# Optimization experiments

Hardware: AMD Instinct MI355X
Metric: run time of the kernel (lower is better)

Reference implementation:

```python
import jax, jax.numpy as jnp
import numpy as np

HI, WI = 56, 56
HO, WO = HI // 2, WI // 2
N_IN, N_OUT = HI * WI, HO * WO
DIM_IN, DIM_OUT = 96, 192
HIDDEN = DIM_OUT * 2
NUM_ITERS = 3
LN_EPS = 1e-5


def _build_mask_and_qidx():
    # M_loc: 0 inside 3x3 window around each input token's parent slot, -1e4 outside.
    # qidx: relative-position index in {0..8}, -1 outside window (torch rpb[-1] == rpb[8]).
    mask = np.full((N_IN, N_OUT), -10000.0, dtype=np.float32)
    qidx = np.full((N_IN, N_OUT), -1, dtype=np.int32)
    in_r, in_c = np.meshgrid(np.arange(HI), np.arange(WI), indexing='ij')
    in_r, in_c = in_r.ravel(), in_c.ravel()
    out_r0 = np.clip(in_r // 2, 0, HO - 1)
    out_c0 = np.clip(in_c // 2, 0, WO - 1)
    in_idx = np.arange(N_IN)
    k = 0
    for dr in (-1, 0, 1):
        for dc in (-1, 0, 1):
            out_r = np.clip(out_r0 + dr, 0, HO - 1)
            out_c = np.clip(out_c0 + dc, 0, WO - 1)
            out_idx = out_r * WO + out_c
            mask[in_idx, out_idx] = 0.0
            qidx[in_idx, out_idx] = k
            k += 1
    return jnp.asarray(mask), jnp.asarray(qidx)


def layer_norm(x, g, b):
    mu = jnp.mean(x, axis=-1, keepdims=True)
    var = jnp.var(x, axis=-1, keepdims=True)
    return (x - mu) * jax.lax.rsqrt(var + LN_EPS) * g + b


def setup_inputs() -> dict:
    key = jax.random.key(0)
    ks = jax.random.split(key, 10)
    B = 8
    x = jax.random.normal(ks[0], (B, N_IN, DIM_IN), dtype=jnp.float32)
    # Parameters (torch Linear weight layout [out, in])
    conv_w = jax.random.normal(ks[1], (DIM_OUT, DIM_IN, 3, 3), dtype=jnp.float32) * np.sqrt(2.0 / (DIM_IN * 9))
    q_w = jax.random.normal(ks[2], (DIM_IN, DIM_OUT), dtype=jnp.float32) * (DIM_OUT ** -0.5)
    k_w = jax.random.normal(ks[3], (DIM_IN, DIM_IN), dtype=jnp.float32) * (DIM_IN ** -0.5)
    v_w = jax.random.normal(ks[4], (DIM_OUT, DIM_IN), dtype=jnp.float32) * (DIM_IN ** -0.5)
    mlp_w1 = jax.random.normal(ks[5], (HIDDEN, DIM_OUT), dtype=jnp.float32) * (DIM_OUT ** -0.5)
    mlp_b1 = jnp.zeros((HIDDEN,), dtype=jnp.float32)
    mlp_w2 = jax.random.normal(ks[6], (DIM_OUT, HIDDEN), dtype=jnp.float32) * (HIDDEN ** -0.5)
    mlp_b2 = jnp.zeros((DIM_OUT,), dtype=jnp.float32)
    ln_in_g = jnp.ones((DIM_IN,), jnp.float32); ln_in_b = jnp.zeros((DIM_IN,), jnp.float32)
    ln_out_g = jnp.ones((DIM_OUT,), jnp.float32); ln_out_b = jnp.zeros((DIM_OUT,), jnp.float32)
    ln_attn_g = jnp.ones((DIM_OUT,), jnp.float32); ln_attn_b = jnp.zeros((DIM_OUT,), jnp.float32)
    ln_mlp_g = jnp.ones((DIM_OUT,), jnp.float32); ln_mlp_b = jnp.zeros((DIM_OUT,), jnp.float32)
    tau = jnp.asarray(np.log(DIM_IN ** -0.5), dtype=jnp.float32)
    rpb = jax.random.truncated_normal(ks[7], -2.0, 2.0, (9,), dtype=jnp.float32) * 0.02
    M_loc, qidx = _build_mask_and_qidx()
    return dict(x=x, conv_w=conv_w, q_w=q_w, k_w=k_w, v_w=v_w,
                mlp_w1=mlp_w1, mlp_b1=mlp_b1, mlp_w2=mlp_w2, mlp_b2=mlp_b2,
                ln_in_g=ln_in_g, ln_in_b=ln_in_b, ln_out_g=ln_out_g, ln_out_b=ln_out_b,
                ln_attn_g=ln_attn_g, ln_attn_b=ln_attn_b, ln_mlp_g=ln_mlp_g, ln_mlp_b=ln_mlp_b,
                tau=tau, rpb=rpb, M_loc=M_loc, qidx=qidx)


def reference(x, conv_w, q_w, k_w, v_w, mlp_w1, mlp_b1, mlp_w2, mlp_b2,
              ln_in_g, ln_in_b, ln_out_g, ln_out_b, ln_attn_g, ln_attn_b,
              ln_mlp_g, ln_mlp_b, tau, rpb, M_loc, qidx):
    B = x.shape[0]
    # seed: strided 3x3 conv (stride 2, pad 1), NCHW
    x_img = jnp.transpose(x, (0, 2, 1)).reshape(B, DIM_IN, HI, WI)
    seed = jax.lax.conv_general_dilated(
        x_img, conv_w, window_strides=(2, 2), padding=((1, 1), (1, 1)),
        dimension_numbers=('NCHW', 'OIHW', 'NCHW'))  # [B, dim_out, Ho, Wo]
    x_out = layer_norm(jnp.transpose(seed.reshape(B, DIM_OUT, N_OUT), (0, 2, 1)), ln_out_g, ln_out_b)
    xn = layer_norm(x, ln_in_g, ln_in_b)
    k = xn @ k_w.T  # [B, N_in, dim_in]
    v = xn @ v_w.T  # [B, N_in, dim_out]
    # relative-position bias gather; torch index -1 wraps to 8
    bias = rpb[jnp.where(qidx < 0, qidx + 9, qidx)]  # [N_in, N_out]
    add = bias + M_loc  # fused constant-per-batch additive term
    a_ups = a_down = None
    for _ in range(NUM_ITERS):
        q = layer_norm(x_out, ln_out_g, ln_out_b) @ q_w.T  # [B, N_out, dim_in]
        logits = jnp.einsum('bnd,bmd->bnm', k, q) * jnp.exp(tau) + add
        a_ups = jax.nn.softmax(logits, axis=-1)          # row softmax over slots
        col_sums = jnp.sum(a_ups, axis=1, keepdims=True)  # column renorm (Sinkhorn-like)
        a_down = a_ups / (col_sums + 1e-8)
        updates = jnp.einsum('bnm,bnd->bmd', a_down, v)   # [B, N_out, dim_out]
        x_out = x_out + layer_norm(updates, ln_attn_g, ln_attn_b)
        h = jax.nn.gelu(x_out @ mlp_w1.T + mlp_b1, approximate=False) @ mlp_w2.T + mlp_b2
        x_out = x_out + layer_norm(h, ln_mlp_g, ln_mlp_b)
    return x_out, a_ups, a_down
```

## Files before the change

kernel.cpp:

```cpp
#include <hip/hip_runtime.h>
#include <hip/hip_bf16.h>
#include <math.h>

#define NB 8
#define NIN 3136
#define NOUT 784
#define DIN 96
#define DOUT 192
#define HID 384
#define TOK_IN (NB*NIN)
#define TOK_OUT (NB*NOUT)

__device__ __forceinline__ void window9(int n, int* ms, bool* dup) {
  int r = n / 56, c = n % 56;
  int rb = r >> 1, cb = c >> 1;
  #pragma unroll
  for (int j = 0; j < 9; j++) {
    int ro = rb + (j/3) - 1; ro = ro < 0 ? 0 : (ro > 27 ? 27 : ro);
    int co = cb + (j%3) - 1; co = co < 0 ? 0 : (co > 27 ? 27 : co);
    ms[j] = ro*28 + co;
  }
  #pragma unroll
  for (int j = 0; j < 9; j++) {
    bool d = false;
    #pragma unroll
    for (int i = 0; i < j; i++) d = d || (ms[i] == ms[j]);
    dup[j] = d;
  }
}

__global__ void k_tr(const float* __restrict__ cw, const float* __restrict__ kw,
                     const float* __restrict__ vw, const float* __restrict__ qw,
                     const float* __restrict__ w1, const float* __restrict__ w2,
                     const float* __restrict__ rpb, const int* __restrict__ qidx,
                     float* __restrict__ wct, float* __restrict__ wkv4, float* __restrict__ qw4,
                     float* __restrict__ w1_4, float* __restrict__ w2_4,
                     float* __restrict__ bias9) {
  int i = blockIdx.x * 256 + threadIdx.x;
  if (i < 165888) {
    int q = i & 3; int t1 = i >> 2;
    int co = t1 % 192; int t2 = t1 / 192;
    int kwi = t2 % 3; int t3 = t2 / 3;
    int ci4m = t3 % 6; int t4 = t3 / 6;
    int kh = t4 % 3; int ch = t4 / 3;
    wct[i] = cw[((co*96 + ch*24 + ci4m*4 + q)*3 + kh)*3 + kwi];
  } else if (i < 165888 + 27648) {
    int j = i - 165888; int q = j & 3; int rest = j >> 2;
    int o = rest % 288; int e = (rest / 288)*4 + q;
    wkv4[j] = (o < 96) ? kw[o*96 + e] : vw[(o-96)*96 + e];
  } else if (i < 165888 + 27648 + 18432) {
    int j = i - 165888 - 27648; int q = j & 3; int rest = j >> 2;
    int o = rest % 96; int e = (rest / 96)*4 + q;
    qw4[j] = qw[o*192 + e];
  } else if (i < 165888 + 27648 + 18432 + 73728) {
    int j = i - 165888 - 27648 - 18432; int q = j & 3; int rest = j >> 2;
    int hh = rest % 384; int e = (rest / 384)*4 + q;
    w1_4[j] = w1[hh*192 + e];
  } else if (i < 165888 + 27648 + 18432 + 73728 + 73728) {
    int j = i - 165888 - 27648 - 18432 - 73728; int q = j & 3; int rest = j >> 2;
    int o = rest % 192; int h = (rest / 192)*4 + q;
    w2_4[j] = w2[o*384 + h];
  } else if (i < 165888 + 27648 + 18432 + 73728 + 73728 + 28224) {
    int j = i - 165888 - 27648 - 18432 - 73728 - 73728;
    int j9 = j % 9; int n = j / 9;
    int ms[9]; bool dup[9];
    window9(n, ms, dup);
    bias9[j] = rpb[qidx[(size_t)n*NOUT + ms[j9]]];
  }
}

__global__ __launch_bounds__(224, 4) void k_conv(const float* __restrict__ x,
                                                 const float* __restrict__ wct,
                                                 float* __restrict__ s0, float* __restrict__ s1,
                                                 float* __restrict__ s2, float* __restrict__ s3) {
  __shared__ float xs[3][58][24];
  int ho = blockIdx.x;
  int half = blockIdx.y & 1, ch = blockIdx.y >> 1;
  int b = blockIdx.z;
  int t = threadIdx.x;
  const float* xb0 = x + (size_t)b*NIN*DIN + ch*24;
  for (int i = t; i < 3*58*6; i += 224) {
    int q = i % 6; int rest = i / 6;
    int col = rest % 58; int kh = rest / 58;
    int h = 2*ho - 1 + kh, c = col - 1;
    float4 v = make_float4(0.f,0.f,0.f,0.f);
    if (h >= 0 && h < 56 && c >= 0 && c < 56)
      v = *(const float4*)(xb0 + ((size_t)h*56 + c)*DIN + q*4);
    *(float4*)&xs[kh][col][q*4] = v;
  }
  __syncthreads();
  int ol = t & 31, tg = t >> 5;
  int co = half*96 + ol;
  float acc[4][3];
  #pragma unroll
  for (int i = 0; i < 4; i++) { acc[i][0]=0.f; acc[i][1]=0.f; acc[i][2]=0.f; }
  #pragma unroll
  for (int kh = 0; kh < 3; kh++) {
    const float4* wp = (const float4*)wct + (size_t)(ch*3 + kh)*3456 + co;
    const float* xb = &xs[kh][8*tg][0];
    #pragma unroll
    for (int ci4 = 0; ci4 < 6; ci4++) {
      float4 xr[9];
      #pragma unroll
      for (int c = 0; c < 9; c++) xr[c] = *(const float4*)(xb + c*24);
      #pragma unroll
      for (int kwv = 0; kwv < 3; kwv++) {
        float4 w0 = wp[kwv*192], w1 = wp[kwv*192 + 32], w2 = wp[kwv*192 + 64];
        #pragma unroll
        for (int i = 0; i < 4; i++) {
          float4 xv = xr[2*i + kwv];
          acc[i][0] += xv.x*w0.x + xv.y*w0.y + xv.z*w0.z + xv.w*w0.w;
          acc[i][1] += xv.x*w1.x + xv.y*w1.y + xv.z*w1.z + xv.w*w1.w;
          acc[i][2] += xv.x*w2.x + xv.y*w2.y + xv.z*w2.z + xv.w*w2.w;
        }
      }
      wp += 576; xb += 4;
    }
  }
  float* sp = (ch == 0) ? s0 : (ch == 1) ? s1 : (ch == 2) ? s2 : s3;
  #pragma unroll
  for (int i = 0; i < 4; i++)
    #pragma unroll
    for (int j = 0; j < 3; j++)
      sp[((size_t)b*NOUT + ho*28 + 4*tg + i)*DOUT + co + 32*j] = acc[i][j];
}

__global__ __launch_bounds__(256) void k_lnq(const float* __restrict__ s0, const float* __restrict__ s1,
                                             const float* __restrict__ s2, const float* __restrict__ s3,
                                             const float* __restrict__ qw4,
                                             const float* __restrict__ lng, const float* __restrict__ lnb,
                                             float* __restrict__ xo, float* __restrict__ qb) {
  __shared__ float xt[16][196];
  int tok0 = blockIdx.x * 16;
  int t = threadIdx.x;
  int tok16 = t >> 4, l16 = t & 15;
  size_t base = (size_t)(tok0 + tok16)*DOUT;
  float v[12], s = 0.f, sq = 0.f;
  #pragma unroll
  for (int j = 0; j < 12; j++) {
    int e = l16 + 16*j;
    float vv = s0[base + e] + s1[base + e] + s2[base + e] + s3[base + e];
    v[j] = vv; s += vv; sq += vv*vv;
  }
  #pragma unroll
  for (int off = 8; off; off >>= 1) { s += __shfl_xor(s, off, 16); sq += __shfl_xor(sq, off, 16); }
  float mu = s * (1.f/192.f);
  float var = sq * (1.f/192.f) - mu*mu;
  float rs = rsqrtf(var + 1e-5f);
  float s2a = 0.f, sq2 = 0.f;
  #pragma unroll
  for (int j = 0; j < 12; j++) {
    int e = l16 + 16*j;
    float y = (v[j]-mu)*rs*lng[e] + lnb[e];
    xo[base + e] = y;
    v[j] = y; s2a += y; sq2 += y*y;
  }
  #pragma unroll
  for (int off = 8; off; off >>= 1) { s2a += __shfl_xor(s2a, off, 16); sq2 += __shfl_xor(sq2, off, 16); }
  float mu2 = s2a * (1.f/192.f);
  float var2 = sq2 * (1.f/192.f) - mu2*mu2;
  float rs2 = rsqrtf(var2 + 1e-5f);
  #pragma unroll
  for (int j = 0; j < 12; j++) {
    int e = l16 + 16*j;
    xt[tok16][e] = (v[j]-mu2)*rs2*lng[e] + lnb[e];
  }
  __syncthreads();
  int ol = t & 31, tg = t >> 5;
  float acc[2][3];
  #pragma unroll
  for (int i = 0; i < 2; i++) { acc[i][0]=0.f; acc[i][1]=0.f; acc[i][2]=0.f; }
  const float4* wp = (const float4*)qw4 + ol;
  for (int e4 = 0; e4 < 48; e4++) {
    float4 w0 = wp[0], w1 = wp[32], w2 = wp[64];
    #pragma unroll
    for (int i = 0; i < 2; i++) {
      float4 xv = *(const float4*)&xt[tg*2+i][e4*4];
      acc[i][0] += xv.x*w0.x + xv.y*w0.y + xv.z*w0.z + xv.w*w0.w;
      acc[i][1] += xv.x*w1.x + xv.y*w1.y + xv.z*w1.z + xv.w*w1.w;
      acc[i][2] += xv.x*w2.x + xv.y*w2.y + xv.z*w2.z + xv.w*w2.w;
    }
    wp += 96;
  }
  #pragma unroll
  for (int i = 0; i < 2; i++)
    #pragma unroll
    for (int j = 0; j < 3; j++)
      qb[(size_t)(tok0 + tg*2 + i)*DIN + ol + 32*j] = acc[i][j];
}

__global__ __launch_bounds__(256) void k_kv(const float* __restrict__ x,
                                            const float* __restrict__ wkv4,
                                            const float* __restrict__ lng, const float* __restrict__ lnb,
                                            float* __restrict__ kvb) {
  __shared__ float xt[32][100];
  int tok0 = blockIdx.x * 32;
  int t = threadIdx.x;
  const float4* xp = (const float4*)(x + (size_t)tok0*DIN);
  for (int i = t; i < 32*24; i += 256) {
    int tok = i / 24, q = i % 24;
    *(float4*)&xt[tok][q*4] = xp[i];
  }
  __syncthreads();
  int tok8 = t >> 3, l8 = t & 7;
  float vv[12], s = 0.f, sq = 0.f;
  #pragma unroll
  for (int j = 0; j < 12; j++) {
    float v = xt[tok8][l8 + 8*j];
    vv[j] = v; s += v; sq += v*v;
  }
  #pragma unroll
  for (int off = 4; off; off >>= 1) { s += __shfl_xor(s, off, 8); sq += __shfl_xor(sq, off, 8); }
  float mu = s * (1.f/96.f);
  float var = sq * (1.f/96.f) - mu*mu;
  float rs = rsqrtf(var + 1e-5f);
  #pragma unroll
  for (int j = 0; j < 12; j++) {
    int e = l8 + 8*j;
    xt[tok8][e] = (vv[j]-mu)*rs*lng[e] + lnb[e];
  }
  __syncthreads();
  int ol = t & 31, tg = t >> 5;
  float acc[4][9];
  #pragma unroll
  for (int i = 0; i < 4; i++)
    #pragma unroll
    for (int j = 0; j < 9; j++) acc[i][j] = 0.f;
  const float4* wp = (const float4*)wkv4 + ol;
  for (int e4 = 0; e4 < 24; e4++) {
    float4 w[9];
    #pragma unroll
    for (int j = 0; j < 9; j++) w[j] = wp[32*j];
    #pragma unroll
    for (int i = 0; i < 4; i++) {
      float4 xv = *(const float4*)&xt[tg*4+i][e4*4];
      #pragma unroll
      for (int j = 0; j < 9; j++)
        acc[i][j] += xv.x*w[j].x + xv.y*w[j].y + xv.z*w[j].z + xv.w*w[j].w;
    }
    wp += 288;
  }
  #pragma unroll
  for (int i = 0; i < 4; i++)
    #pragma unroll
    for (int j = 0; j < 9; j++)
      kvb[(size_t)(tok0 + tg*4 + i)*288 + ol + 32*j] = acc[i][j];
}

__global__ __launch_bounds__(256) void k_attn1(const float* __restrict__ kvb,
                                               const float* __restrict__ qb,
                                               const float* __restrict__ tau,
                                               const float* __restrict__ bias9,
                                               float* __restrict__ aups,
                                               float* __restrict__ adown, int zmode) {
  int t = threadIdx.x;
  int half = (t >> 5) & 1, ll = t & 31;
  int tid = blockIdx.x * 8 + (t >> 6) * 2 + half;
  int b = tid / NIN, n = tid % NIN;
  int ms[9]; bool dup[9];
  window9(n, ms, dup);
  const float* kp = kvb + (size_t)tid * 288;
  float k0 = kp[ll], k1 = kp[32 + ll], k2 = kp[64 + ll];
  float et = expf(tau[0]);
  float p[9];
  #pragma unroll
  for (int j = 0; j < 9; j++) {
    const float* qp = qb + (size_t)(b*NOUT + ms[j]) * DIN;
    p[j] = k0 * qp[ll] + k1 * qp[32 + ll] + k2 * qp[64 + ll];
  }
  #pragma unroll
  for (int off = 16; off; off >>= 1)
    #pragma unroll
    for (int j = 0; j < 9; j++) p[j] += __shfl_xor(p[j], off, 32);
  const float* bp = bias9 + (size_t)n*9;
  float lg[9];
  #pragma unroll
  for (int j = 0; j < 9; j++)
    lg[j] = dup[j] ? -1e30f : p[j] * et + bp[j];
  float mx = lg[0];
  #pragma unroll
  for (int j = 1; j < 9; j++) mx = fmaxf(mx, lg[j]);
  float s = 0.f, ex[9];
  #pragma unroll
  for (int j = 0; j < 9; j++) { ex[j] = dup[j] ? 0.f : expf(lg[j] - mx); s += ex[j]; }
  float inv = 1.0f / s;
  if (zmode) {
    float* ap = aups + (size_t)tid*NOUT;
    float* dp = adown + (size_t)tid*NOUT;
    #pragma unroll
    for (int k = 0; k < 25; k++) {
      int e = ll + 32*k;
      if (e < NOUT) {
        float v = 0.f;
        #pragma unroll
        for (int j = 0; j < 9; j++)
          if (!dup[j] && e == ms[j]) v = ex[j] * inv;
        ap[e] = v;
        dp[e] = 0.f;
      }
    }
  } else {
    #pragma unroll
    for (int j = 0; j < 9; j++) {
      if (ll == j && !dup[j])
        aups[(size_t)tid*NOUT + ms[j]] = ex[j] * inv;
    }
  }
}

__global__ __launch_bounds__(192) void k_upd(const float* __restrict__ aups,
                                             const float* __restrict__ kvb,
                                             float* __restrict__ xout,
                                             const float* __restrict__ g,
                                             const float* __restrict__ bb,
                                             float* __restrict__ adown, int wadown) {
  __shared__ float avals[4][64];
  __shared__ float red[4][3][2];
  __shared__ float bc[4][2];
  __shared__ float csv[4];
  int b = blockIdx.z;
  int ro0 = blockIdx.y*2, co0 = blockIdx.x*2;
  int r0 = 2*ro0 - 2; if (r0 < 0) r0 = 0;
  int r1 = 2*ro0 + 5; if (r1 > 55) r1 = 55;
  int c0 = 2*co0 - 2; if (c0 < 0) c0 = 0;
  int c1 = 2*co0 + 5; if (c1 > 55) c1 = 55;
  int nr = r1 - r0 + 1, nc = c1 - c0 + 1, cnt = nr*nc;
  int t = threadIdx.x;
  int m0 = ro0*28 + co0, m1 = m0+1, m2 = m0+28, m3 = m0+29;
  if (t < cnt) {
    int ri = t / nc, ci = t % nc;
    int n = (r0 + ri)*56 + (c0 + ci);
    const float* ap = aups + ((size_t)b*NIN + n)*NOUT;
    avals[0][t] = ap[m0]; avals[1][t] = ap[m1];
    avals[2][t] = ap[m2]; avals[3][t] = ap[m3];
  } else if (t < 64) {
    avals[0][t] = 0.f; avals[1][t] = 0.f; avals[2][t] = 0.f; avals[3][t] = 0.f;
  }
  __syncthreads();
  if (t < 64) {
    float cv0 = avals[0][t], cv1 = avals[1][t], cv2 = avals[2][t], cv3 = avals[3][t];
    #pragma unroll
    for (int off = 32; off; off >>= 1) {
      cv0 += __shfl_xor(cv0, off); cv1 += __shfl_xor(cv1, off);
      cv2 += __shfl_xor(cv2, off); cv3 += __shfl_xor(cv3, off);
    }
    if (t == 0) { csv[0]=cv0; csv[1]=cv1; csv[2]=cv2; csv[3]=cv3; }
  }
  __syncthreads();
  float a0=0.f, a1=0.f, a2=0.f, a3=0.f;
  int i = 0;
  for (int ri = 0; ri < nr; ri++) {
    int nbase = (r0 + ri)*56 + c0;
    for (int ci = 0; ci < nc; ci++, i++) {
      float vv = kvb[((size_t)b*NIN + nbase + ci)*288 + 96 + t];
      a0 += avals[0][i]*vv; a1 += avals[1][i]*vv;
      a2 += avals[2][i]*vv; a3 += avals[3][i]*vv;
    }
  }
  float inv0 = 1.0f/(csv[0]+1e-8f);
  float inv1 = 1.0f/(csv[1]+1e-8f);
  float inv2 = 1.0f/(csv[2]+1e-8f);
  float inv3 = 1.0f/(csv[3]+1e-8f);
  if (wadown && t < cnt) {
    int ri = t / nc, ci = t % nc;
    int n = (r0 + ri)*56 + (c0 + ci);
    float* dp = adown + ((size_t)b*NIN + n)*NOUT;
    dp[m0] = avals[0][t]*inv0; dp[m1] = avals[1][t]*inv1;
    dp[m2] = avals[2][t]*inv2; dp[m3] = avals[3][t]*inv3;
  }
  a0 *= inv0; a1 *= inv1; a2 *= inv2; a3 *= inv3;
  float s0=a0,s1=a1,s2=a2,s3=a3, q0=a0*a0,q1=a1*a1,q2=a2*a2,q3=a3*a3;
  #pragma unroll
  for (int off = 32; off; off >>= 1) {
    s0 += __shfl_xor(s0, off); q0 += __shfl_xor(q0, off);
    s1 += __shfl_xor(s1, off); q1 += __shfl_xor(q1, off);
    s2 += __shfl_xor(s2, off); q2 += __shfl_xor(q2, off);
    s3 += __shfl_xor(s3, off); q3 += __shfl_xor(q3, off);
  }
  int w = t >> 6, l = t & 63;
  if (l == 0) {
    red[0][w][0]=s0; red[0][w][1]=q0;
    red[1][w][0]=s1; red[1][w][1]=q1;
    red[2][w][0]=s2; red[2][w][1]=q2;
    red[3][w][0]=s3; red[3][w][1]=q3;
  }
  __syncthreads();
  if (t < 4) {
    float S = red[t][0][0]+red[t][1][0]+red[t][2][0];
    float Q = red[t][0][1]+red[t][1][1]+red[t][2][1];
    float mu = S * (1.0f/192.0f);
    float var = Q * (1.0f/192.0f) - mu*mu;
    bc[t][0] = mu; bc[t][1] = rsqrtf(var + 1e-5f);
  }
  __syncthreads();
  float gt = g[t], bt = bb[t];
  xout[((size_t)b*NOUT+m0)*DOUT + t] += (a0-bc[0][0])*bc[0][1]*gt + bt;
  xout[((size_t)b*NOUT+m1)*DOUT + t] += (a1-bc[1][0])*bc[1][1]*gt + bt;
  xout[((size_t)b*NOUT+m2)*DOUT + t] += (a2-bc[2][0])*bc[2][1]*gt + bt;
  xout[((size_t)b*NOUT+m3)*DOUT + t] += (a3-bc[3][0])*bc[3][1]*gt + bt;
}

__global__ __launch_bounds__(256) void k_mlp1(const float* __restrict__ xout,
                                              const float* __restrict__ w1_4, const float* __restrict__ b1,
                                              float* __restrict__ ht) {
  __shared__ float xt[32][196];
  int tok0 = blockIdx.x * 32;
  int h0 = blockIdx.y * 96;
  int t = threadIdx.x;
  const float4* xp = (const float4*)(xout + (size_t)tok0*DOUT);
  for (int i = t; i < 32*48; i += 256) {
    int tok = i / 48, q = i % 48;
    *(float4*)&xt[tok][q*4] = xp[i];
  }
  __syncthreads();
  int ol = t & 31, tg = t >> 5;
  float acc[4][3];
  #pragma unroll
  for (int i = 0; i < 4; i++) { acc[i][0]=0.f; acc[i][1]=0.f; acc[i][2]=0.f; }
  const float4* wp = (const float4*)w1_4 + h0 + ol;
  for (int e4 = 0; e4 < 48; e4++) {
    float4 w0 = wp[0], w1v = wp[32], w2v = wp[64];
    #pragma unroll
    for (int i = 0; i < 4; i++) {
      float4 xv = *(const float4*)&xt[tg*4+i][e4*4];
      acc[i][0] += xv.x*w0.x + xv.y*w0.y + xv.z*w0.z + xv.w*w0.w;
      acc[i][1] += xv.x*w1v.x + xv.y*w1v.y + xv.z*w1v.z + xv.w*w1v.w;
      acc[i][2] += xv.x*w2v.x + xv.y*w2v.y + xv.z*w2v.z + xv.w*w2v.w;
    }
    wp += 384;
  }
  #pragma unroll
  for (int j = 0; j < 3; j++) {
    int hh = h0 + ol + 32*j;
    float bv = b1[hh];
    #pragma unroll
    for (int i = 0; i < 4; i++) {
      float v = acc[i][j] + bv;
      v = 0.5f*v*(1.0f + erff(v*0.70710678118f));
      ht[(size_t)(tok0 + tg*4 + i)*HID + hh] = v;
    }
  }
}

__global__ __launch_bounds__(256) void k_mlpq(float* __restrict__ xout,
                                              const float* __restrict__ ht,
                                              const float* __restrict__ w2_4, const float* __restrict__ b2,
                                              const float* __restrict__ g, const float* __restrict__ bb,
                                              const float* __restrict__ qw4,
                                              const float* __restrict__ lng, const float* __restrict__ lnb,
                                              float* __restrict__ qb,
                                              float* __restrict__ dout, int last) {
  __shared__ float hs[16][388];
  __shared__ float xt[16][196];
  int tok0 = blockIdx.x * 16;
  int t = threadIdx.x;
  const float4* hp = (const float4*)(ht + (size_t)tok0*HID);
  for (int i = t; i < 16*96; i += 256) {
    int tok = i / 96, q = i % 96;
    *(float4*)&hs[tok][q*4] = hp[i];
  }
  __syncthreads();
  int ol = t & 31, tg = t >> 5;
  float acc[2][6];
  #pragma unroll
  for (int i = 0; i < 2; i++)
    #pragma unroll
    for (int j = 0; j < 6; j++) acc[i][j] = 0.f;
  const float4* wp = (const float4*)w2_4 + ol;
  for (int h4 = 0; h4 < 96; h4++) {
    float4 w[6];
    #pragma unroll
    for (int j = 0; j < 6; j++) w[j] = wp[32*j];
    #pragma unroll
    for (int i = 0; i < 2; i++) {
      float4 hv = *(const float4*)&hs[tg*2+i][h4*4];
      #pragma unroll
      for (int j = 0; j < 6; j++)
        acc[i][j] += hv.x*w[j].x + hv.y*w[j].y + hv.z*w[j].z + hv.w*w[j].w;
    }
    wp += 192;
  }
  #pragma unroll
  for (int i = 0; i < 2; i++) {
    int tl = tg*2 + i;
    int tok = tok0 + tl;
    float v[6], s = 0.f, sq = 0.f;
    #pragma unroll
    for (int j = 0; j < 6; j++) {
      v[j] = acc[i][j] + b2[ol + 32*j];
      s += v[j]; sq += v[j]*v[j];
    }
    #pragma unroll
    for (int off = 16; off; off >>= 1) { s += __shfl_xor(s, off, 32); sq += __shfl_xor(sq, off, 32); }
    float mu = s * (1.f/192.f);
    float var = sq * (1.f/192.f) - mu*mu;
    float rs = rsqrtf(var + 1e-5f);
    #pragma unroll
    for (int j = 0; j < 6; j++) {
      int o = ol + 32*j;
      float nv = (v[j] - mu)*rs*g[o] + bb[o];
      size_t gi = (size_t)tok*DOUT + o;
      float nx = xout[gi] + nv;
      xout[gi] = nx;
      if (last) dout[gi] = nx;
      xt[tl][o] = nx;
    }
  }
  if (last) return;
  __syncthreads();
  {
    int tok16 = t >> 4, l16 = t & 15;
    float vv[12], s = 0.f, sq = 0.f;
    #pragma unroll
    for (int j = 0; j < 12; j++) {
      float v = xt[tok16][l16 + 16*j];
      vv[j] = v; s += v; sq += v*v;
    }
    #pragma unroll
    for (int off = 8; off; off >>= 1) { s += __shfl_xor(s, off, 16); sq += __shfl_xor(sq, off, 16); }
    float mu = s * (1.f/192.f);
    float var = sq * (1.f/192.f) - mu*mu;
    float rs = rsqrtf(var + 1e-5f);
    __syncthreads();
    #pragma unroll
    for (int j = 0; j < 12; j++) {
      int e = l16 + 16*j;
      xt[tok16][e] = (vv[j]-mu)*rs*lng[e] + lnb[e];
    }
  }
  __syncthreads();
  float qa[2][3];
  #pragma unroll
  for (int i = 0; i < 2; i++) { qa[i][0]=0.f; qa[i][1]=0.f; qa[i][2]=0.f; }
  const float4* qp = (const float4*)qw4 + ol;
  for (int e4 = 0; e4 < 48; e4++) {
    float4 w0 = qp[0], w1 = qp[32], w2 = qp[64];
    #pragma unroll
    for (int i = 0; i < 2; i++) {
      float4 xv = *(const float4*)&xt[tg*2+i][e4*4];
      qa[i][0] += xv.x*w0.x + xv.y*w0.y + xv.z*w0.z + xv.w*w0.w;
      qa[i][1] += xv.x*w1.x + xv.y*w1.y + xv.z*w1.z + xv.w*w1.w;
      qa[i][2] += xv.x*w2.x + xv.y*w2.y + xv.z*w2.z + xv.w*w2.w;
    }
    qp += 96;
  }
  #pragma unroll
  for (int i = 0; i < 2; i++)
    #pragma unroll
    for (int j = 0; j < 3; j++)
      qb[(size_t)(tok0 + tg*2 + i)*DIN + ol + 32*j] = qa[i][j];
}

extern "C" void kernel_launch(void* const* d_in, const int* in_sizes, int n_in,
                              void* d_out, int out_size, void* d_ws, size_t ws_size,
                              hipStream_t stream) {
  (void)in_sizes; (void)n_in; (void)ws_size; (void)out_size;
  const float* x        = (const float*)d_in[0];
  const float* conv_w   = (const float*)d_in[1];
  const float* q_w      = (const float*)d_in[2];
  const float* k_w      = (const float*)d_in[3];
  const float* v_w      = (const float*)d_in[4];
  const float* mlp_w1   = (const float*)d_in[5];
  const float* mlp_b1   = (const float*)d_in[6];
  const float* mlp_w2   = (const float*)d_in[7];
  const float* mlp_b2   = (const float*)d_in[8];
  const float* ln_in_g  = (const float*)d_in[9];
  const float* ln_in_b  = (const float*)d_in[10];
  const float* ln_out_g = (const float*)d_in[11];
  const float* ln_out_b = (const float*)d_in[12];
  const float* ln_attn_g= (const float*)d_in[13];
  const float* ln_attn_b= (const float*)d_in[14];
  const float* ln_mlp_g = (const float*)d_in[15];
  const float* ln_mlp_b = (const float*)d_in[16];
  const float* tau      = (const float*)d_in[17];
  const float* rpb      = (const float*)d_in[18];
  const int*   qidx     = (const int*)d_in[20];

  float* out = (float*)d_out;
  float* aups  = out + 1204224;
  float* adown = out + 20873216;

  float* ws   = (float*)d_ws;
  float* wct  = ws;
  float* wkv4 = wct + 165888;
  float* qw4  = wkv4 + 27648;
  float* w1_4 = qw4 + 18432;
  float* w2_4 = w1_4 + 73728;
  float* bias9= w2_4 + 73728;
  float* kvb  = bias9 + 28224;
  float* seed0= kvb + (size_t)TOK_IN*288;
  float* seed1= seed0 + (size_t)TOK_OUT*DOUT;
  float* seed2= seed1 + (size_t)TOK_OUT*DOUT;
  float* seed3= seed2 + (size_t)TOK_OUT*DOUT;
  float* xo   = seed3 + (size_t)TOK_OUT*DOUT;
  float* qb   = xo + (size_t)TOK_OUT*DOUT;
  float* htb  = seed0;

  k_tr<<<1515, 256, 0, stream>>>(conv_w, k_w, v_w, q_w, mlp_w1, mlp_w2, rpb, qidx,
                                 wct, wkv4, qw4, w1_4, w2_4, bias9);
  k_conv<<<dim3(28, 8, 8), 224, 0, stream>>>(x, wct, seed0, seed1, seed2, seed3);
  k_lnq<<<TOK_OUT/16, 256, 0, stream>>>(seed0, seed1, seed2, seed3, qw4,
                                        ln_out_g, ln_out_b, xo, qb);
  k_kv<<<TOK_IN/32, 256, 0, stream>>>(x, wkv4, ln_in_g, ln_in_b, kvb);

  for (int it = 0; it < 3; it++) {
    k_attn1<<<TOK_IN/8, 256, 0, stream>>>(kvb, qb, tau, bias9, aups, adown, it == 0);
    k_upd<<<dim3(14, 14, NB), 192, 0, stream>>>(aups, kvb, xo, ln_attn_g, ln_attn_b,
                                                adown, it == 2);
    k_mlp1<<<dim3(TOK_OUT/32, 4), 256, 0, stream>>>(xo, w1_4, mlp_b1, htb);
    k_mlpq<<<TOK_OUT/16, 256, 0, stream>>>(xo, htb, w2_4, mlp_b2,
                                           ln_mlp_g, ln_mlp_b,
                                           qw4, ln_out_g, ln_out_b, qb,
                                           out, it == 2);
  }
}
```

Measured before the change: 777.8 us.

## Fuse MLP first and second layers into one kernel keeping hidden in LDS

```diff
diff --git a/kernel.cpp b/kernel.cpp
--- a/kernel.cpp
+++ b/kernel.cpp
@@ -400,155 +400,107 @@
   xout[((size_t)b*NOUT+m3)*DOUT + t] += (a3-bc[3][0])*bc[3][1]*gt + bt;
 }
 
-__global__ __launch_bounds__(256) void k_mlp1(const float* __restrict__ xout,
+__global__ __launch_bounds__(256) void k_mlpf(float* __restrict__ xout,
                                               const float* __restrict__ w1_4, const float* __restrict__ b1,
-                                              float* __restrict__ ht) {
-  __shared__ float xt[32][196];
-  int tok0 = blockIdx.x * 32;
-  int h0 = blockIdx.y * 96;
-  int t = threadIdx.x;
-  const float4* xp = (const float4*)(xout + (size_t)tok0*DOUT);
-  for (int i = t; i < 32*48; i += 256) {
-    int tok = i / 48, q = i % 48;
-    *(float4*)&xt[tok][q*4] = xp[i];
-  }
-  __syncthreads();
-  int ol = t & 31, tg = t >> 5;
-  float acc[4][3];
-  #pragma unroll
-  for (int i = 0; i < 4; i++) { acc[i][0]=0.f; acc[i][1]=0.f; acc[i][2]=0.f; }
-  const float4* wp = (const float4*)w1_4 + h0 + ol;
-  for (int e4 = 0; e4 < 48; e4++) {
-    float4 w0 = wp[0], w1v = wp[32], w2v = wp[64];
-    #pragma unroll
-    for (int i = 0; i < 4; i++) {
-      float4 xv = *(const float4*)&xt[tg*4+i][e4*4];
-      acc[i][0] += xv.x*w0.x + xv.y*w0.y + xv.z*w0.z + xv.w*w0.w;
-      acc[i][1] += xv.x*w1v.x + xv.y*w1v.y + xv.z*w1v.z + xv.w*w1v.w;
-      acc[i][2] += xv.x*w2v.x + xv.y*w2v.y + xv.z*w2v.z + xv.w*w2v.w;
-    }
-    wp += 384;
-  }
-  #pragma unroll
-  for (int j = 0; j < 3; j++) {
-    int hh = h0 + ol + 32*j;
-    float bv = b1[hh];
-    #pragma unroll
-    for (int i = 0; i < 4; i++) {
-      float v = acc[i][j] + bv;
-      v = 0.5f*v*(1.0f + erff(v*0.70710678118f));
-      ht[(size_t)(tok0 + tg*4 + i)*HID + hh] = v;
-    }
-  }
-}
-
-__global__ __launch_bounds__(256) void k_mlpq(float* __restrict__ xout,
-                                              const float* __restrict__ ht,
                                               const float* __restrict__ w2_4, const float* __restrict__ b2,
-                                              const float* __restrict__ g, const float* __restrict__ bb,
+                                              const float* __restrict__ gm, const float* __restrict__ bm,
                                               const float* __restrict__ qw4,
                                               const float* __restrict__ lng, const float* __restrict__ lnb,
                                               float* __restrict__ qb,
                                               float* __restrict__ dout, int last) {
-  __shared__ float hs[16][388];
-  __shared__ float xt[16][196];
-  int tok0 = blockIdx.x * 16;
+  __shared__ float xt[8][196];
+  __shared__ float ht[8][388];
+  int tok0 = blockIdx.x * 8;
   int t = threadIdx.x;
-  const float4* hp = (const float4*)(ht + (size_t)tok0*HID);
-  for (int i = t; i < 16*96; i += 256) {
-    int tok = i / 96, q = i % 96;
-    *(float4*)&hs[tok][q*4] = hp[i];
+  const float4* xp = (const float4*)(xout + (size_t)tok0*DOUT);
+  for (int i = t; i < 8*48; i += 256) {
+    int tok = i / 48, q = i % 48;
+    *(float4*)&xt[tok][q*4] = xp[i];
   }
   __syncthreads();
   int ol = t & 31, tg = t >> 5;
-  float acc[2][6];
-  #pragma unroll
-  for (int i = 0; i < 2; i++)
-    #pragma unroll
-    for (int j = 0; j < 6; j++) acc[i][j] = 0.f;
-  const float4* wp = (const float4*)w2_4 + ol;
+  float acc[12];
+  #pragma unroll
+  for (int j = 0; j < 12; j++) acc[j] = 0.f;
+  const float4* wp = (const float4*)w1_4 + ol;
+  for (int e4 = 0; e4 < 48; e4++) {
+    float4 xv = *(const float4*)&xt[tg][e4*4];
+    #pragma unroll
+    for (int j = 0; j < 12; j++) {
+      float4 w = wp[32*j];
+      acc[j] += xv.x*w.x + xv.y*w.y + xv.z*w.z + xv.w*w.w;
+    }
+    wp += 384;
+  }
+  #pragma unroll
+  for (int j = 0; j < 12; j++) {
+    int hh = ol + 32*j;
+    float v = acc[j] + b1[hh];
+    v = 0.5f*v*(1.0f + erff(v*0.70710678118f));
+    ht[tg][hh] = v;
+  }
+  __syncthreads();
+  float o2[6];
+  #pragma unroll
+  for (int j = 0; j < 6; j++) o2[j] = 0.f;
+  const float4* w2p = (const float4*)w2_4 + ol;
   for (int h4 = 0; h4 < 96; h4++) {
-    float4 w[6];
-    #pragma unroll
-    for (int j = 0; j < 6; j++) w[j] = wp[32*j];
-    #pragma unroll
-    for (int i = 0; i < 2; i++) {
-      float4 hv = *(const float4*)&hs[tg*2+i][h4*4];
-      #pragma unroll
-      for (int j = 0; j < 6; j++)
-        acc[i][j] += hv.x*w[j].x + hv.y*w[j].y + hv.z*w[j].z + hv.w*w[j].w;
-    }
-    wp += 192;
-  }
-  #pragma unroll
-  for (int i = 0; i < 2; i++) {
-    int tl = tg*2 + i;
-    int tok = tok0 + tl;
-    float v[6], s = 0.f, sq = 0.f;
+    float4 hv = *(const float4*)&ht[tg][h4*4];
     #pragma unroll
     for (int j = 0; j < 6; j++) {
-      v[j] = acc[i][j] + b2[ol + 32*j];
-      s += v[j]; sq += v[j]*v[j];
-    }
-    #pragma unroll
-    for (int off = 16; off; off >>= 1) { s += __shfl_xor(s, off, 32); sq += __shfl_xor(sq, off, 32); }
-    float mu = s * (1.f/192.f);
-    float var = sq * (1.f/192.f) - mu*mu;
-    float rs = rsqrtf(var + 1e-5f);
-    #pragma unroll
-    for (int j = 0; j < 6; j++) {
-      int o = ol + 32*j;
-      float nv = (v[j] - mu)*rs*g[o] + bb[o];
-      size_t gi = (size_t)tok*DOUT + o;
-      float nx = xout[gi] + nv;
-      xout[gi] = nx;
-      if (last) dout[gi] = nx;
-      xt[tl][o] = nx;
-    }
+      float4 w = w2p[32*j];
+      o2[j] += hv.x*w.x + hv.y*w.y + hv.z*w.z + hv.w*w.w;
+    }
+    w2p += 192;
+  }
+  float v[6], s = 0.f, sq = 0.f;
+  #pragma unroll
+  for (int j = 0; j < 6; j++) {
+    v[j] = o2[j] + b2[ol + 32*j];
+    s += v[j]; sq += v[j]*v[j];
+  }
+  #pragma unroll
+  for (int off = 16; off; off >>= 1) { s += __shfl_xor(s, off, 32); sq += __shfl_xor(sq, off, 32); }
+  float mu = s * (1.f/192.f);
+  float var = sq * (1.f/192.f) - mu*mu;
+  float rs = rsqrtf(var + 1e-5f);
+  float nx6[6], s2 = 0.f, sq2 = 0.f;
+  #pragma unroll
+  for (int j = 0; j < 6; j++) {
+    int o = ol + 32*j;
+    float nv = (v[j] - mu)*rs*gm[o] + bm[o];
+    size_t gi = (size_t)(tok0 + tg)*DOUT + o;
+    float nx = xout[gi] + nv;
+    xout[gi] = nx;
+    if (last) dout[gi] = nx;
+    nx6[j] = nx; s2 += nx; sq2 += nx*nx;
   }
   if (last) return;
-  __syncthreads();
-  {
-    int tok16 = t >> 4, l16 = t & 15;
-    float vv[12], s = 0.f, sq = 0.f;
-    #pragma unroll
-    for (int j = 0; j < 12; j++) {
-      float v = xt[tok16][l16 + 16*j];
-      vv[j] = v; s += v; sq += v*v;
-    }
-    #pragma unroll
-    for (int off = 8; off; off >>= 1) { s += __shfl_xor(s, off, 16); sq += __shfl_xor(sq, off, 16); }
-    float mu = s * (1.f/192.f);
-    float var = sq * (1.f/192.f) - mu*mu;
-    float rs = rsqrtf(var + 1e-5f);
-    __syncthreads();
-    #pragma unroll
-    for (int j = 0; j < 12; j++) {
-      int e = l16 + 16*j;
-      xt[tok16][e] = (vv[j]-mu)*rs*lng[e] + lnb[e];
-    }
-  }
-  __syncthreads();
-  float qa[2][3];
-  #pragma unroll
-  for (int i = 0; i < 2; i++) { qa[i][0]=0.f; qa[i][1]=0.f; qa[i][2]=0.f; }
+  #pragma unroll
+  for (int off = 16; off; off >>= 1) { s2 += __shfl_xor(s2, off, 32); sq2 += __shfl_xor(sq2, off, 32); }
+  float mu2 = s2 * (1.f/192.f);
+  float var2 = sq2 * (1.f/192.f) - mu2*mu2;
+  float rs2 = rsqrtf(var2 + 1e-5f);
+  #pragma unroll
+  for (int j = 0; j < 6; j++) {
+    int o = ol + 32*j;
+    ht[tg][o] = (nx6[j] - mu2)*rs2*lng[o] + lnb[o];
+  }
+  __syncthreads();
+  float qa[3] = {0.f, 0.f, 0.f};
   const float4* qp = (const float4*)qw4 + ol;
   for (int e4 = 0; e4 < 48; e4++) {
-    float4 w0 = qp[0], w1 = qp[32], w2 = qp[64];
-    #pragma unroll
-    for (int i = 0; i < 2; i++) {
-      float4 xv = *(const float4*)&xt[tg*2+i][e4*4];
-      qa[i][0] += xv.x*w0.x + xv.y*w0.y + xv.z*w0.z + xv.w*w0.w;
-      qa[i][1] += xv.x*w1.x + xv.y*w1.y + xv.z*w1.z + xv.w*w1.w;
-      qa[i][2] += xv.x*w2.x + xv.y*w2.y + xv.z*w2.z + xv.w*w2.w;
+    float4 xv = *(const float4*)&ht[tg][e4*4];
+    #pragma unroll
+    for (int j = 0; j < 3; j++) {
+      float4 w = qp[32*j];
+      qa[j] += xv.x*w.x + xv.y*w.y + xv.z*w.z + xv.w*w.w;
     }
     qp += 96;
   }
   #pragma unroll
-  for (int i = 0; i < 2; i++)
-    #pragma unroll
-    for (int j = 0; j < 3; j++)
-      qb[(size_t)(tok0 + tg*2 + i)*DIN + ol + 32*j] = qa[i][j];
+  for (int j = 0; j < 3; j++)
+    qb[(size_t)(tok0 + tg)*DIN + ol + 32*j] = qa[j];
 }
 
 extern "C" void kernel_launch(void* const* d_in, const int* in_sizes, int n_in,
@@ -594,7 +546,6 @@
   float* seed3= seed2 + (size_t)TOK_OUT*DOUT;
   float* xo   = seed3 + (size_t)TOK_OUT*DOUT;
   float* qb   = xo + (size_t)TOK_OUT*DOUT;
-  float* htb  = seed0;
 
   k_tr<<<1515, 256, 0, stream>>>(conv_w, k_w, v_w, q_w, mlp_w1, mlp_w2, rpb, qidx,
                                  wct, wkv4, qw4, w1_4, w2_4, bias9);
@@ -607,10 +558,9 @@
     k_attn1<<<TOK_IN/8, 256, 0, stream>>>(kvb, qb, tau, bias9, aups, adown, it == 0);
     k_upd<<<dim3(14, 14, NB), 192, 0, stream>>>(aups, kvb, xo, ln_attn_g, ln_attn_b,
                                                 adown, it == 2);
-    k_mlp1<<<dim3(TOK_OUT/32, 4), 256, 0, stream>>>(xo, w1_4, mlp_b1, htb);
-    k_mlpq<<<TOK_OUT/16, 256, 0, stream>>>(xo, htb, w2_4, mlp_b2,
-                                           ln_mlp_g, ln_mlp_b,
-                                           qw4, ln_out_g, ln_out_b, qb,
-                                           out, it == 2);
-  }
-}
+    k_mlpf<<<TOK_OUT/8, 256, 0, stream>>>(xo, w1_4, mlp_b1, w2_4, mlp_b2,
+                                          ln_mlp_g, ln_mlp_b,
+                                          qw4, ln_out_g, ln_out_b, qb,
+                                          out, it == 2);
+  }
+}
```

New measurement: 845.5 us. 1.09x slower.

## Fold q projection into keys: precompute k·Wq so attention dots normalized x_out directly

Applied to the files above, without the earlier changes.

```diff
diff --git a/kernel.cpp b/kernel.cpp
--- a/kernel.cpp
+++ b/kernel.cpp
@@ -33,7 +33,8 @@
                      const float* __restrict__ vw, const float* __restrict__ qw,
                      const float* __restrict__ w1, const float* __restrict__ w2,
                      const float* __restrict__ rpb, const int* __restrict__ qidx,
-                     float* __restrict__ wct, float* __restrict__ wkv4, float* __restrict__ qw4,
+                     float* __restrict__ wct, float* __restrict__ kw4, float* __restrict__ vw4,
+                     float* __restrict__ qwt4,
                      float* __restrict__ w1_4, float* __restrict__ w2_4,
                      float* __restrict__ bias9) {
   int i = blockIdx.x * 256 + threadIdx.x;
@@ -44,24 +45,28 @@
     int ci4m = t3 % 6; int t4 = t3 / 6;
     int kh = t4 % 3; int ch = t4 / 3;
     wct[i] = cw[((co*96 + ch*24 + ci4m*4 + q)*3 + kh)*3 + kwi];
-  } else if (i < 165888 + 27648) {
+  } else if (i < 175104) {
     int j = i - 165888; int q = j & 3; int rest = j >> 2;
-    int o = rest % 288; int e = (rest / 288)*4 + q;
-    wkv4[j] = (o < 96) ? kw[o*96 + e] : vw[(o-96)*96 + e];
-  } else if (i < 165888 + 27648 + 18432) {
-    int j = i - 165888 - 27648; int q = j & 3; int rest = j >> 2;
-    int o = rest % 96; int e = (rest / 96)*4 + q;
-    qw4[j] = qw[o*192 + e];
-  } else if (i < 165888 + 27648 + 18432 + 73728) {
-    int j = i - 165888 - 27648 - 18432; int q = j & 3; int rest = j >> 2;
+    int o = rest % 96; int e4 = rest / 96;
+    kw4[j] = kw[o*96 + e4*4 + q];
+  } else if (i < 193536) {
+    int j = i - 175104; int q = j & 3; int rest = j >> 2;
+    int o = rest % 192; int e4 = rest / 192;
+    vw4[j] = vw[o*96 + e4*4 + q];
+  } else if (i < 211968) {
+    int j = i - 193536; int q = j & 3; int rest = j >> 2;
+    int e = rest % 192; int d4 = rest / 192;
+    qwt4[j] = qw[(d4*4 + q)*192 + e];
+  } else if (i < 285696) {
+    int j = i - 211968; int q = j & 3; int rest = j >> 2;
     int hh = rest % 384; int e = (rest / 384)*4 + q;
     w1_4[j] = w1[hh*192 + e];
-  } else if (i < 165888 + 27648 + 18432 + 73728 + 73728) {
-    int j = i - 165888 - 27648 - 18432 - 73728; int q = j & 3; int rest = j >> 2;
+  } else if (i < 359424) {
+    int j = i - 285696; int q = j & 3; int rest = j >> 2;
     int o = rest % 192; int h = (rest / 192)*4 + q;
     w2_4[j] = w2[o*384 + h];
-  } else if (i < 165888 + 27648 + 18432 + 73728 + 73728 + 28224) {
-    int j = i - 165888 - 27648 - 18432 - 73728 - 73728;
+  } else if (i < 387648) {
+    int j = i - 359424;
     int j9 = j % 9; int n = j / 9;
     int ms[9]; bool dup[9];
     window9(n, ms, dup);
@@ -127,10 +132,8 @@
 
 __global__ __launch_bounds__(256) void k_lnq(const float* __restrict__ s0, const float* __restrict__ s1,
                                              const float* __restrict__ s2, const float* __restrict__ s3,
-                                             const float* __restrict__ qw4,
                                              const float* __restrict__ lng, const float* __restrict__ lnb,
-                                             float* __restrict__ xo, float* __restrict__ qb) {
-  __shared__ float xt[16][196];
+                                             float* __restrict__ xo, float* __restrict__ xqn) {
   int tok0 = blockIdx.x * 16;
   int t = threadIdx.x;
   int tok16 = t >> 4, l16 = t & 15;
@@ -163,37 +166,17 @@
   #pragma unroll
   for (int j = 0; j < 12; j++) {
     int e = l16 + 16*j;
-    xt[tok16][e] = (v[j]-mu2)*rs2*lng[e] + lnb[e];
-  }
-  __syncthreads();
-  int ol = t & 31, tg = t >> 5;
-  float acc[2][3];
-  #pragma unroll
-  for (int i = 0; i < 2; i++) { acc[i][0]=0.f; acc[i][1]=0.f; acc[i][2]=0.f; }
-  const float4* wp = (const float4*)qw4 + ol;
-  for (int e4 = 0; e4 < 48; e4++) {
-    float4 w0 = wp[0], w1 = wp[32], w2 = wp[64];
-    #pragma unroll
-    for (int i = 0; i < 2; i++) {
-      float4 xv = *(const float4*)&xt[tg*2+i][e4*4];
-      acc[i][0] += xv.x*w0.x + xv.y*w0.y + xv.z*w0.z + xv.w*w0.w;
-      acc[i][1] += xv.x*w1.x + xv.y*w1.y + xv.z*w1.z + xv.w*w1.w;
-      acc[i][2] += xv.x*w2.x + xv.y*w2.y + xv.z*w2.z + xv.w*w2.w;
-    }
-    wp += 96;
-  }
-  #pragma unroll
-  for (int i = 0; i < 2; i++)
-    #pragma unroll
-    for (int j = 0; j < 3; j++)
-      qb[(size_t)(tok0 + tg*2 + i)*DIN + ol + 32*j] = acc[i][j];
+    xqn[base + e] = (v[j]-mu2)*rs2*lng[e] + lnb[e];
+  }
 }
 
 __global__ __launch_bounds__(256) void k_kv(const float* __restrict__ x,
-                                            const float* __restrict__ wkv4,
+                                            const float* __restrict__ kw4, const float* __restrict__ vw4,
+                                            const float* __restrict__ qwt4,
                                             const float* __restrict__ lng, const float* __restrict__ lnb,
                                             float* __restrict__ kvb) {
   __shared__ float xt[32][100];
+  __shared__ float ks[32][100];
   int tok0 = blockIdx.x * 32;
   int t = threadIdx.x;
   const float4* xp = (const float4*)(x + (size_t)tok0*DIN);
@@ -221,34 +204,78 @@
   }
   __syncthreads();
   int ol = t & 31, tg = t >> 5;
-  float acc[4][9];
+  float ak[4][3];
+  #pragma unroll
+  for (int i = 0; i < 4; i++) { ak[i][0]=0.f; ak[i][1]=0.f; ak[i][2]=0.f; }
+  const float4* kp = (const float4*)kw4 + ol;
+  for (int e4 = 0; e4 < 24; e4++) {
+    float4 w0 = kp[0], w1 = kp[32], w2 = kp[64];
+    #pragma unroll
+    for (int i = 0; i < 4; i++) {
+      float4 xv = *(const float4*)&xt[tg*4+i][e4*4];
+      ak[i][0] += xv.x*w0.x + xv.y*w0.y + xv.z*w0.z + xv.w*w0.w;
+      ak[i][1] += xv.x*w1.x + xv.y*w1.y + xv.z*w1.z + xv.w*w1.w;
+      ak[i][2] += xv.x*w2.x + xv.y*w2.y + xv.z*w2.z + xv.w*w2.w;
+    }
+    kp += 96;
+  }
   #pragma unroll
   for (int i = 0; i < 4; i++)
     #pragma unroll
-    for (int j = 0; j < 9; j++) acc[i][j] = 0.f;
-  const float4* wp = (const float4*)wkv4 + ol;
+    for (int j = 0; j < 3; j++)
+      ks[tg*4+i][ol + 32*j] = ak[i][j];
+  __syncthreads();
+  float akt[4][6];
+  #pragma unroll
+  for (int i = 0; i < 4; i++)
+    #pragma unroll
+    for (int j = 0; j < 6; j++) akt[i][j] = 0.f;
+  const float4* qp = (const float4*)qwt4 + ol;
+  for (int d4 = 0; d4 < 24; d4++) {
+    float4 w[6];
+    #pragma unroll
+    for (int j = 0; j < 6; j++) w[j] = qp[32*j];
+    #pragma unroll
+    for (int i = 0; i < 4; i++) {
+      float4 kv4 = *(const float4*)&ks[tg*4+i][d4*4];
+      #pragma unroll
+      for (int j = 0; j < 6; j++)
+        akt[i][j] += kv4.x*w[j].x + kv4.y*w[j].y + kv4.z*w[j].z + kv4.w*w[j].w;
+    }
+    qp += 192;
+  }
+  float av[4][6];
+  #pragma unroll
+  for (int i = 0; i < 4; i++)
+    #pragma unroll
+    for (int j = 0; j < 6; j++) av[i][j] = 0.f;
+  const float4* vp = (const float4*)vw4 + ol;
   for (int e4 = 0; e4 < 24; e4++) {
-    float4 w[9];
-    #pragma unroll
-    for (int j = 0; j < 9; j++) w[j] = wp[32*j];
+    float4 w[6];
+    #pragma unroll
+    for (int j = 0; j < 6; j++) w[j] = vp[32*j];
     #pragma unroll
     for (int i = 0; i < 4; i++) {
       float4 xv = *(const float4*)&xt[tg*4+i][e4*4];
       #pragma unroll
-      for (int j = 0; j < 9; j++)
-        acc[i][j] += xv.x*w[j].x + xv.y*w[j].y + xv.z*w[j].z + xv.w*w[j].w;
-    }
-    wp += 288;
-  }
-  #pragma unroll
-  for (int i = 0; i < 4; i++)
-    #pragma unroll
-    for (int j = 0; j < 9; j++)
-      kvb[(size_t)(tok0 + tg*4 + i)*288 + ol + 32*j] = acc[i][j];
+      for (int j = 0; j < 6; j++)
+        av[i][j] += xv.x*w[j].x + xv.y*w[j].y + xv.z*w[j].z + xv.w*w[j].w;
+    }
+    vp += 192;
+  }
+  #pragma unroll
+  for (int i = 0; i < 4; i++) {
+    float* op = kvb + (size_t)(tok0 + tg*4 + i)*384;
+    #pragma unroll
+    for (int j = 0; j < 6; j++) {
+      op[ol + 32*j] = akt[i][j];
+      op[192 + ol + 32*j] = av[i][j];
+    }
+  }
 }
 
 __global__ __launch_bounds__(256) void k_attn1(const float* __restrict__ kvb,
-                                               const float* __restrict__ qb,
+                                               const float* __restrict__ xqn,
                                                const float* __restrict__ tau,
                                                const float* __restrict__ bias9,
                                                float* __restrict__ aups,
@@ -259,14 +286,19 @@
   int b = tid / NIN, n = tid % NIN;
   int ms[9]; bool dup[9];
   window9(n, ms, dup);
-  const float* kp = kvb + (size_t)tid * 288;
-  float k0 = kp[ll], k1 = kp[32 + ll], k2 = kp[64 + ll];
+  const float* kp = kvb + (size_t)tid * 384;
+  float kt[6];
+  #pragma unroll
+  for (int j6 = 0; j6 < 6; j6++) kt[j6] = kp[ll + 32*j6];
   float et = expf(tau[0]);
   float p[9];
   #pragma unroll
   for (int j = 0; j < 9; j++) {
-    const float* qp = qb + (size_t)(b*NOUT + ms[j]) * DIN;
-    p[j] = k0 * qp[ll] + k1 * qp[32 + ll] + k2 * qp[64 + ll];
+    const float* qp = xqn + (size_t)(b*NOUT + ms[j]) * DOUT;
+    float pv = 0.f;
+    #pragma unroll
+    for (int j6 = 0; j6 < 6; j6++) pv += kt[j6] * qp[ll + 32*j6];
+    p[j] = pv;
   }
   #pragma unroll
   for (int off = 16; off; off >>= 1)
@@ -352,7 +384,7 @@
   for (int ri = 0; ri < nr; ri++) {
     int nbase = (r0 + ri)*56 + c0;
     for (int ci = 0; ci < nc; ci++, i++) {
-      float vv = kvb[((size_t)b*NIN + nbase + ci)*288 + 96 + t];
+      float vv = kvb[((size_t)b*NIN + nbase + ci)*384 + 192 + t];
       a0 += avals[0][i]*vv; a1 += avals[1][i]*vv;
       a2 += avals[2][i]*vv; a3 += avals[3][i]*vv;
     }
@@ -446,12 +478,10 @@
                                               const float* __restrict__ ht,
                                               const float* __restrict__ w2_4, const float* __restrict__ b2,
                                               const float* __restrict__ g, const float* __restrict__ bb,
-                                              const float* __restrict__ qw4,
                                               const float* __restrict__ lng, const float* __restrict__ lnb,
-                                              float* __restrict__ qb,
+                                              float* __restrict__ xqn,
                                               float* __restrict__ dout, int last) {
   __shared__ float hs[16][388];
-  __shared__ float xt[16][196];
   int tok0 = blockIdx.x * 16;
   int t = threadIdx.x;
   const float4* hp = (const float4*)(ht + (size_t)tok0*HID);
@@ -482,8 +512,7 @@
   }
   #pragma unroll
   for (int i = 0; i < 2; i++) {
-    int tl = tg*2 + i;
-    int tok = tok0 + tl;
+    int tok = tok0 + tg*2 + i;
     float v[6], s = 0.f, sq = 0.f;
     #pragma unroll
     for (int j = 0; j < 6; j++) {
@@ -495,6 +524,7 @@
     float mu = s * (1.f/192.f);
     float var = sq * (1.f/192.f) - mu*mu;
     float rs = rsqrtf(var + 1e-5f);
+    float nx6[6], s2 = 0.f, sq2 = 0.f;
     #pragma unroll
     for (int j = 0; j < 6; j++) {
       int o = ol + 32*j;
@@ -503,52 +533,21 @@
       float nx = xout[gi] + nv;
       xout[gi] = nx;
       if (last) dout[gi] = nx;
-      xt[tl][o] = nx;
-    }
-  }
-  if (last) return;
-  __syncthreads();
-  {
-    int tok16 = t >> 4, l16 = t & 15;
-    float vv[12], s = 0.f, sq = 0.f;
-    #pragma unroll
-    for (int j = 0; j < 12; j++) {
-      float v = xt[tok16][l16 + 16*j];
-      vv[j] = v; s += v; sq += v*v;
-    }
-    #pragma unroll
-    for (int off = 8; off; off >>= 1) { s += __shfl_xor(s, off, 16); sq += __shfl_xor(sq, off, 16); }
-    float mu = s * (1.f/192.f);
-    float var = sq * (1.f/192.f) - mu*mu;
-    float rs = rsqrtf(var + 1e-5f);
-    __syncthreads();
-    #pragma unroll
-    for (int j = 0; j < 12; j++) {
-      int e = l16 + 16*j;
-      xt[tok16][e] = (vv[j]-mu)*rs*lng[e] + lnb[e];
-    }
-  }
-  __syncthreads();
-  float qa[2][3];
-  #pragma unroll
-  for (int i = 0; i < 2; i++) { qa[i][0]=0.f; qa[i][1]=0.f; qa[i][2]=0.f; }
-  const float4* qp = (const float4*)qw4 + ol;
-  for (int e4 = 0; e4 < 48; e4++) {
-    float4 w0 = qp[0], w1 = qp[32], w2 = qp[64];
-    #pragma unroll
-    for (int i = 0; i < 2; i++) {
-      float4 xv = *(const float4*)&xt[tg*2+i][e4*4];
-      qa[i][0] += xv.x*w0.x + xv.y*w0.y + xv.z*w0.z + xv.w*w0.w;
-      qa[i][1] += xv.x*w1.x + xv.y*w1.y + xv.z*w1.z + xv.w*w1.w;
-      qa[i][2] += xv.x*w2.x + xv.y*w2.y + xv.z*w2.z + xv.w*w2.w;
-    }
-    qp += 96;
-  }
-  #pragma unroll
-  for (int i = 0; i < 2; i++)
-    #pragma unroll
-    for (int j = 0; j < 3; j++)
-      qb[(size_t)(tok0 + tg*2 + i)*DIN + ol + 32*j] = qa[i][j];
+      nx6[j] = nx; s2 += nx; sq2 += nx*nx;
+    }
+    if (!last) {
+      #pragma unroll
+      for (int off = 16; off; off >>= 1) { s2 += __shfl_xor(s2, off, 32); sq2 += __shfl_xor(sq2, off, 32); }
+      float mu2 = s2 * (1.f/192.f);
+      float var2 = sq2 * (1.f/192.f) - mu2*mu2;
+      float rs2 = rsqrtf(var2 + 1e-5f);
+      #pragma unroll
+      for (int j = 0; j < 6; j++) {
+        int o = ol + 32*j;
+        xqn[(size_t)tok*DOUT + o] = (nx6[j] - mu2)*rs2*lng[o] + lnb[o];
+      }
+    }
+  }
 }
 
 extern "C" void kernel_launch(void* const* d_in, const int* in_sizes, int n_in,
@@ -582,35 +581,36 @@
 
   float* ws   = (float*)d_ws;
   float* wct  = ws;
-  float* wkv4 = wct + 165888;
-  float* qw4  = wkv4 + 27648;
-  float* w1_4 = qw4 + 18432;
+  float* kw4  = wct + 165888;
+  float* vw4  = kw4 + 9216;
+  float* qwt4 = vw4 + 18432;
+  float* w1_4 = qwt4 + 18432;
   float* w2_4 = w1_4 + 73728;
   float* bias9= w2_4 + 73728;
   float* kvb  = bias9 + 28224;
-  float* seed0= kvb + (size_t)TOK_IN*288;
+  float* seed0= kvb + (size_t)TOK_IN*384;
   float* seed1= seed0 + (size_t)TOK_OUT*DOUT;
   float* seed2= seed1 + (size_t)TOK_OUT*DOUT;
   float* seed3= seed2 + (size_t)TOK_OUT*DOUT;
   float* xo   = seed3 + (size_t)TOK_OUT*DOUT;
-  float* qb   = xo + (size_t)TOK_OUT*DOUT;
+  float* xqn  = xo + (size_t)TOK_OUT*DOUT;
   float* htb  = seed0;
 
   k_tr<<<1515, 256, 0, stream>>>(conv_w, k_w, v_w, q_w, mlp_w1, mlp_w2, rpb, qidx,
-                                 wct, wkv4, qw4, w1_4, w2_4, bias9);
+                                 wct, kw4, vw4, qwt4, w1_4, w2_4, bias9);
   k_conv<<<dim3(28, 8, 8), 224, 0, stream>>>(x, wct, seed0, seed1, seed2, seed3);
-  k_lnq<<<TOK_OUT/16, 256, 0, stream>>>(seed0, seed1, seed2, seed3, qw4,
-                                        ln_out_g, ln_out_b, xo, qb);
-  k_kv<<<TOK_IN/32, 256, 0, stream>>>(x, wkv4, ln_in_g, ln_in_b, kvb);
+  k_lnq<<<TOK_OUT/16, 256, 0, stream>>>(seed0, seed1, seed2, seed3,
+                                        ln_out_g, ln_out_b, xo, xqn);
+  k_kv<<<TOK_IN/32, 256, 0, stream>>>(x, kw4, vw4, qwt4, ln_in_g, ln_in_b, kvb);
 
   for (int it = 0; it < 3; it++) {
-    k_attn1<<<TOK_IN/8, 256, 0, stream>>>(kvb, qb, tau, bias9, aups, adown, it == 0);
+    k_attn1<<<TOK_IN/8, 256, 0, stream>>>(kvb, xqn, tau, bias9, aups, adown, it == 0);
     k_upd<<<dim3(14, 14, NB), 192, 0, stream>>>(aups, kvb, xo, ln_attn_g, ln_attn_b,
                                                 adown, it == 2);
     k_mlp1<<<dim3(TOK_OUT/32, 4), 256, 0, stream>>>(xo, w1_4, mlp_b1, htb);
     k_mlpq<<<TOK_OUT/16, 256, 0, stream>>>(xo, htb, w2_4, mlp_b2,
                                            ln_mlp_g, ln_mlp_b,
-                                           qw4, ln_out_g, ln_out_b, qb,
+                                           ln_out_g, ln_out_b, xqn,
                                            out, it == 2);
   }
 }
```

New measurement: 660.2 us. 15.1% less time.
